# Kernel tuning notes

Hardware: AMD Instinct MI355X
Metric: run time of the kernel (lower is better)

Reference implementation:

```python
import jax, jax.numpy as jnp
import numpy as np

B, P, D = 256, 128, 768        # batch, property slots per sample, encoder hidden dim
E = 64                          # num_properties (number of adapter heads)
H = 256                         # adapter_hidden_dim
H2 = H // 2
O = 2                           # output_dim
LN_EPS = 1e-5
RES_W_ADPT, RES_W_BASE = 0.7, 0.3


def setup_inputs() -> dict:
    key = jax.random.key(0)
    ks = jax.random.split(key, 12)
    hidden_states = jax.random.normal(ks[0], (B, P, D), dtype=jnp.float32)
    base_output = jax.random.normal(ks[1], (B, P, O), dtype=jnp.float32)
    properties = jax.random.randint(ks[2], (B, P), 0, E, dtype=jnp.int64)
    mask = (jax.random.uniform(ks[3], (B, P)) > 0.1).astype(jnp.float32)
    # Stacked per-head adapter parameters (LayerNorm + 3 Linears per head)
    ln_g = jnp.ones((E, D), dtype=jnp.float32)
    ln_b = jnp.zeros((E, D), dtype=jnp.float32)
    W1 = jax.random.normal(ks[4], (E, D, H), dtype=jnp.float32) * (1.0 / np.sqrt(D))
    b1 = jnp.zeros((E, H), dtype=jnp.float32)
    W2 = jax.random.normal(ks[5], (E, H, H2), dtype=jnp.float32) * (1.0 / np.sqrt(H))
    b2 = jnp.zeros((E, H2), dtype=jnp.float32)
    W3 = jax.random.normal(ks[6], (E, H2, O), dtype=jnp.float32) * 0.01  # init std=0.01 per source
    b3 = jnp.zeros((E, O), dtype=jnp.float32)
    return {
        "hidden_states": hidden_states, "base_output": base_output,
        "properties": properties, "mask": mask,
        "ln_g": ln_g, "ln_b": ln_b, "W1": W1, "b1": b1,
        "W2": W2, "b2": b2, "W3": W3, "b3": b3,
    }


def reference(hidden_states, base_output, properties, mask,
              ln_g, ln_b, W1, b1, W2, b2, W3, b3):
    b, p, d = hidden_states.shape
    o = W3.shape[-1]
    x = hidden_states.reshape(-1, d)                        # [N, D]
    # LayerNorm statistics are head-independent; only gamma/beta differ per head
    mu = jnp.mean(x, axis=-1, keepdims=True)
    var = jnp.mean((x - mu) ** 2, axis=-1, keepdims=True)
    xhat = (x - mu) * jax.lax.rsqrt(var + LN_EPS)           # [N, D]
    flat_p = properties.reshape(-1)                         # [N]
    flat_m = mask.reshape(-1)                               # [N]

    def body(acc, inp):
        idx, g, bt, w1, bb1, w2, bb2, w3, bb3 = inp
        h = jax.nn.relu((xhat * g + bt) @ w1 + bb1)         # [N, H]  (dropout = identity in eval)
        h = jax.nn.relu(h @ w2 + bb2)                       # [N, H2]
        out = h @ w3 + bb3                                  # [N, O]
        sel = (flat_p == idx) & (flat_m > 0)
        return jnp.where(sel[:, None], out, acc), None

    e = W1.shape[0]
    acc0 = jnp.zeros((b * p, o), dtype=x.dtype)
    acc, _ = jax.lax.scan(
        body, acc0,
        (jnp.arange(e), ln_g, ln_b, W1, b1, W2, b2, W3, b3))
    out = acc.reshape(b, p, o)
    out = RES_W_ADPT * out + RES_W_BASE * base_output       # use_residual=True
    return out * mask[..., None]
```

## Files before the change

### kernel.cpp

```cpp
#include <hip/hip_runtime.h>
#include <stdint.h>

typedef unsigned short u16;
typedef unsigned int   u32;

#define NTOK   32768
#define GD     768
#define GH     256
#define GH2    128
#define GE     64

typedef __bf16 bf16x8 __attribute__((ext_vector_type(8)));
typedef float  f32x4  __attribute__((ext_vector_type(4)));
union Frag { uint4 u; bf16x8 b; };

__device__ __forceinline__ float bf2f(u16 h) {
  union { u32 u; float f; } v; v.u = ((u32)h) << 16; return v.f;
}
__device__ __forceinline__ u16 f2bf(float f) {
  union { float f; u32 u; } v; v.f = f;
  u32 r = (v.u + 0x7fffu + ((v.u >> 16) & 1u)) >> 16;
  return (u16)r;
}

__device__ __forceinline__ void async16(void* lds, const void* g) {
  __builtin_amdgcn_global_load_lds(
      (const __attribute__((address_space(1))) void*)g,
      (__attribute__((address_space(3))) void*)lds, 16, 0, 0);
}

__device__ __forceinline__ int getProp(const int* p32, int t, int is64) {
  return is64 ? p32[2 * t] : p32[t];
}

static const size_t OFF_Y    = 0;
static const size_t OFF_W1T  = 50331648;
static const size_t OFF_W2T  = 75497472;
static const size_t OFF_TOK  = 79691776;
static const size_t OFF_META = 79822848;

__global__ void setup_kernel(const int* __restrict__ prop, const float* __restrict__ mask,
                             u32* __restrict__ outz, int* __restrict__ counts2d,
                             int* __restrict__ cursors_p, int* __restrict__ flagp) {
  __shared__ int h[GE];
  __shared__ int vOr;
  const int b = blockIdx.x;
  const int tid = threadIdx.x;
  outz[b * 512 + tid] = 0u;
  outz[b * 512 + 256 + tid] = 0u;
  if (b < 4) cursors_p[b * 256 + tid] = 0;
  if (tid < GE) h[tid] = 0;
  if (tid == 0) vOr = 0;
  __syncthreads();
  int v = prop[2 * tid + 1] | prop[2 * (tid + 256) + 1];
  if (v) atomicOr(&vOr, 1);
  __syncthreads();
  const int is64 = (vOr == 0) ? 1 : 0;
  if (b == 0 && tid == 0) *flagp = is64;
  const int t = b * 256 + tid;
  if (mask[t] > 0.f) atomicAdd(&h[getProp(prop, t, is64)], 1);
  __syncthreads();
  if (tid < GE) counts2d[b * GE + tid] = h[tid];
}

__global__ void transpose_w1(const float* __restrict__ in, u16* __restrict__ out) {
  __shared__ u16 tl[64][260];
  const int bid = blockIdx.x;
  const int e  = bid / 12, r = bid % 12;
  const int d0 = (r / 4) * 256, h0 = (r % 4) * 64;
  const int tid = threadIdx.x;
  const size_t inMat = (size_t)e * GD * GH;
  const size_t outMat = (size_t)e * GH * GD;
  const int h_l = (tid & 15) * 4, d_l = tid >> 4;
#pragma unroll
  for (int dd = 0; dd < 16; ++dd) {
    const int d = d_l + dd * 16;
    float4 v = *(const float4*)(in + inMat + (size_t)(d0 + d) * GH + h0 + h_l);
    tl[h_l + 0][d] = f2bf(v.x);
    tl[h_l + 1][d] = f2bf(v.y);
    tl[h_l + 2][d] = f2bf(v.z);
    tl[h_l + 3][d] = f2bf(v.w);
  }
  __syncthreads();
  const int wv = tid >> 6, ln = tid & 63;
#pragma unroll
  for (int hh = 0; hh < 16; ++hh) {
    const int h = wv * 16 + hh;
    *(uint2*)(out + outMat + (size_t)(h0 + h) * GD + d0 + ln * 4) =
        *(const uint2*)&tl[h][ln * 4];
  }
}

__global__ void transpose_kernel(const float* __restrict__ in, u16* __restrict__ out,
                                 int R, int C, int tilesC) {
  __shared__ u16 tile[32][33];
  const int tilesPerMat = (R >> 5) * tilesC;
  const int e  = blockIdx.x / tilesPerMat;
  const int t  = blockIdx.x % tilesPerMat;
  const int tr = t / tilesC, tc = t % tilesC;
  const size_t mat = (size_t)e * R * C;
  const int tx = threadIdx.x & 31, ty = threadIdx.x >> 5;
  const int r0 = tr * 32, c0 = tc * 32;
#pragma unroll
  for (int i = 0; i < 32; i += 8)
    tile[ty + i][tx] = f2bf(in[mat + (size_t)(r0 + ty + i) * C + c0 + tx]);
  __syncthreads();
#pragma unroll
  for (int i = 0; i < 32; i += 8)
    out[mat + (size_t)(c0 + ty + i) * R + r0 + tx] = tile[tx][ty + i];
}

__global__ void ln_kernel(const float* __restrict__ hs, const float* __restrict__ g,
                          const float* __restrict__ bta, const int* __restrict__ prop,
                          u16* __restrict__ y, const int* __restrict__ flag) {
  const int wv = threadIdx.x >> 6, ln = threadIdx.x & 63;
  const int t = blockIdx.x * 4 + wv;
  const float* x = hs + (size_t)t * GD;
  float v[12];
  float s = 0.f, sq = 0.f;
#pragma unroll
  for (int c = 0; c < 3; ++c) {
    float4 u = *(const float4*)(x + c * 256 + ln * 4);
    v[c*4+0] = u.x; v[c*4+1] = u.y; v[c*4+2] = u.z; v[c*4+3] = u.w;
    s  += u.x + u.y + u.z + u.w;
    sq += u.x*u.x + u.y*u.y + u.z*u.z + u.w*u.w;
  }
#pragma unroll
  for (int d = 1; d < 64; d <<= 1) { s += __shfl_xor(s, d); sq += __shfl_xor(sq, d); }
  const float mu = s * (1.f / 768.f);
  const float rstd = rsqrtf(sq * (1.f / 768.f) - mu * mu + 1e-5f);
  const int p = getProp(prop, t, *flag);
  const float* gp = g + (size_t)p * GD;
  const float* bp = bta + (size_t)p * GD;
  u16* yp = y + (size_t)t * GD;
#pragma unroll
  for (int c = 0; c < 3; ++c) {
    float4 ug = *(const float4*)(gp + c * 256 + ln * 4);
    float4 ub = *(const float4*)(bp + c * 256 + ln * 4);
    float y0 = (v[c*4+0] - mu) * rstd * ug.x + ub.x;
    float y1 = (v[c*4+1] - mu) * rstd * ug.y + ub.y;
    float y2 = (v[c*4+2] - mu) * rstd * ug.z + ub.z;
    float y3 = (v[c*4+3] - mu) * rstd * ug.w + ub.w;
    uint2 o;
    o.x = (u32)f2bf(y0) | ((u32)f2bf(y1) << 16);
    o.y = (u32)f2bf(y2) | ((u32)f2bf(y3) << 16);
    *(uint2*)(yp + c * 256 + ln * 4) = o;
  }
}

__global__ void scan_kernel(const int* __restrict__ counts2d, int* __restrict__ offsets,
                            int* __restrict__ tileHead, int* __restrict__ tileRow,
                            int* __restrict__ nTilesPtr) {
  const int e = threadIdx.x;
  int c = 0;
  for (int b = 0; b < 128; ++b) c += counts2d[b * GE + e];
  int inc = c;
#pragma unroll
  for (int d = 1; d < 64; d <<= 1) { int n = __shfl_up(inc, d); if (e >= d) inc += n; }
  const int off = inc - c;
  offsets[e] = off;
  if (e == 63) offsets[64] = inc;
  int ntile = (c + 127) >> 7;
  int inct = ntile;
#pragma unroll
  for (int d = 1; d < 64; d <<= 1) { int n = __shfl_up(inct, d); if (e >= d) inct += n; }
  const int tb = inct - ntile;
  for (int j = 0; j < ntile; ++j) { tileHead[tb + j] = e; tileRow[tb + j] = off + j * 128; }
  if (e == 63) *nTilesPtr = inct;
}

__global__ void scatter_kernel(const int* __restrict__ prop, const float* __restrict__ mask,
                               const int* __restrict__ offsets, int* __restrict__ cursors_p,
                               int* __restrict__ tokenIds, const int* __restrict__ flag) {
  __shared__ int h[GE];
  __shared__ int basebin[GE];
  const int tid = threadIdx.x;
  const int t = blockIdx.x * 256 + tid;
  if (tid < GE) h[tid] = 0;
  __syncthreads();
  int p = -1, rank = 0;
  if (mask[t] > 0.f) {
    p = getProp(prop, t, *flag);
    rank = atomicAdd(&h[p], 1);
  }
  __syncthreads();
  if (tid < GE && h[tid] > 0) basebin[tid] = atomicAdd(&cursors_p[tid * 16], h[tid]);
  __syncthreads();
  if (p >= 0) tokenIds[offsets[p] + basebin[p] + rank] = t;
}

__global__ __launch_bounds__(256, 2) void adapter_gemm(
    const u16* __restrict__ y, const u16* __restrict__ w1t, const u16* __restrict__ w2t,
    const float* __restrict__ b1, const float* __restrict__ b2,
    const float* __restrict__ w3, const float* __restrict__ b3,
    const float* __restrict__ base, const float* __restrict__ mask,
    const int* __restrict__ tokenIds, const int* __restrict__ offsets,
    const int* __restrict__ tileHead, const int* __restrict__ tileRow,
    const int* __restrict__ nTilesPtr, float* __restrict__ outp) {
  __shared__ union LU {
    u16 g1[4][4096];
    u16 h[17408];
  } uni;
  __shared__ u16 sB2[2][4096];
  __shared__ float sBias1[256];
  __shared__ float sBias2[128];
  __shared__ float sW3[2][128];
  __shared__ float sB3[2];
  __shared__ int   sTok[128];

  const int tid  = threadIdx.x;
  const int wv   = tid >> 6;
  const int l15  = tid & 15;
  const int quad = (tid & 63) >> 4;
  const int arow = tid >> 2;
  const int koff = (tid & 3) * 8;
  const f32x4 vzero = {0.f, 0.f, 0.f, 0.f};
  const int nt = *nTilesPtr;

  for (int tile = blockIdx.x; tile < nt; tile += gridDim.x) {
    __syncthreads();
    const int e  = tileHead[tile];
    const int rs = tileRow[tile];
    const int nRows = min(128, offsets[e + 1] - rs);

    if (tid < 128) sTok[tid] = tokenIds[rs + min(tid, nRows - 1)];
    sBias1[tid] = b1[e * GH + tid];
    if (tid < 128) sBias2[tid] = b2[e * GH2 + tid];
    { const int k = tid >> 1, o = tid & 1; sW3[o][k] = w3[e * GH2 * 2 + k * 2 + o]; }
    if (tid < 2) sB3[tid] = b3[e * 2 + tid];
    __syncthreads();

    const u16* yrow0 = y + (size_t)sTok[arow] * GD;
    const u16* yrow1 = y + (size_t)sTok[64 + arow] * GD;
    const u16* w1e = w1t + (size_t)e * GH * GD;
    const u16* w2e = w2t + (size_t)e * GH2 * GH;

    f32x4 acc2[8][2];
#pragma unroll
    for (int f = 0; f < 8; ++f)
#pragma unroll
      for (int g = 0; g < 2; ++g) acc2[f][g] = vzero;

    for (int c = 0; c < 2; ++c) {
      f32x4 acc1[8][2];
#pragma unroll
      for (int f = 0; f < 8; ++f)
#pragma unroll
        for (int g = 0; g < 2; ++g) acc1[f][g] = vzero;

      {
        u16* a = uni.g1[0]; u16* bb = uni.g1[2];
        async16(a + wv * 512,        yrow0 + koff);
        async16(a + 2048 + wv * 512, yrow1 + koff);
#pragma unroll
        for (int j = 0; j < 2; ++j)
          async16(bb + j * 2048 + wv * 512,
                  w1e + (size_t)(c * 128 + j * 64 + arow) * GD + koff);
      }

      for (int kt = 0; kt < 24; ++kt) {
        __syncthreads();
        if (kt + 1 < 24) {
          const int k0 = (kt + 1) * 32;
          const int par = (kt + 1) & 1;
          u16* a = uni.g1[par]; u16* bb = uni.g1[2 + par];
          async16(a + wv * 512,        yrow0 + k0 + koff);
          async16(a + 2048 + wv * 512, yrow1 + k0 + koff);
#pragma unroll
          for (int j = 0; j < 2; ++j)
            async16(bb + j * 2048 + wv * 512,
                    w1e + (size_t)(c * 128 + j * 64 + arow) * GD + k0 + koff);
        }
        const int par = kt & 1;
        const u16* a = uni.g1[par]; const u16* bb = uni.g1[2 + par];
        Frag fa[8], fb[2];
#pragma unroll
        for (int f = 0; f < 8; ++f)
          fa[f].u = *(const uint4*)&a[(f * 16 + l15) * 32 + quad * 8];
#pragma unroll
        for (int g = 0; g < 2; ++g)
          fb[g].u = *(const uint4*)&bb[(wv * 32 + g * 16 + l15) * 32 + quad * 8];
#pragma unroll
        for (int f = 0; f < 8; ++f)
#pragma unroll
          for (int g = 0; g < 2; ++g)
            acc1[f][g] = __builtin_amdgcn_mfma_f32_16x16x32_bf16(fa[f].b, fb[g].b, acc1[f][g], 0, 0, 0);
      }
      __syncthreads();

#pragma unroll
      for (int j = 0; j < 2; ++j)
        async16(sB2[0] + j * 2048 + wv * 512,
                w2e + (size_t)(j * 64 + arow) * GH + c * 128 + koff);

#pragma unroll
      for (int f = 0; f < 8; ++f)
#pragma unroll
        for (int g = 0; g < 2; ++g) {
          const int col = wv * 32 + g * 16 + l15;
          const float bias = sBias1[c * 128 + col];
#pragma unroll
          for (int r = 0; r < 4; ++r) {
            const int row = f * 16 + quad * 4 + r;
            uni.h[row * 136 + col] = f2bf(fmaxf(acc1[f][g][r] + bias, 0.f));
          }
        }

      for (int kt = 0; kt < 4; ++kt) {
        __syncthreads();
        if (kt + 1 < 4) {
          const int k0 = (kt + 1) * 32;
          const int par = (kt + 1) & 1;
#pragma unroll
          for (int j = 0; j < 2; ++j)
            async16(sB2[par] + j * 2048 + wv * 512,
                    w2e + (size_t)(j * 64 + arow) * GH + c * 128 + k0 + koff);
        }
        const int par = kt & 1;
        Frag fa2[8], fb2[2];
#pragma unroll
        for (int f = 0; f < 8; ++f)
          fa2[f].u = *(const uint4*)&uni.h[(f * 16 + l15) * 136 + kt * 32 + quad * 8];
#pragma unroll
        for (int g = 0; g < 2; ++g)
          fb2[g].u = *(const uint4*)&sB2[par][(wv * 32 + g * 16 + l15) * 32 + quad * 8];
#pragma unroll
        for (int f = 0; f < 8; ++f)
#pragma unroll
          for (int g = 0; g < 2; ++g)
            acc2[f][g] = __builtin_amdgcn_mfma_f32_16x16x32_bf16(fa2[f].b, fb2[g].b, acc2[f][g], 0, 0, 0);
      }
      __syncthreads();
    }

#pragma unroll
    for (int f = 0; f < 8; ++f)
#pragma unroll
      for (int g = 0; g < 2; ++g) {
        const int col = wv * 32 + g * 16 + l15;
        const float bias = sBias2[col];
#pragma unroll
        for (int r = 0; r < 4; ++r) {
          const int row = f * 16 + quad * 4 + r;
          uni.h[row * 136 + col] = f2bf(fmaxf(acc2[f][g][r] + bias, 0.f));
        }
      }
    __syncthreads();

    const int m = tid >> 1, o = tid & 1;
    if (m < nRows) {
      float a = sB3[o];
      const u16* h2row = &uni.h[m * 136];
#pragma unroll 16
      for (int k = 0; k < 128; ++k) a += bf2f(h2row[k]) * sW3[o][k];
      const int t = sTok[m];
      const float mk = mask[t];
      const float bs = base[t * 2 + o];
      outp[t * 2 + o] = (0.7f * a + 0.3f * bs) * mk;
    }
  }
}

extern "C" void kernel_launch(void* const* d_in, const int* in_sizes, int n_in,
                              void* d_out, int out_size, void* d_ws, size_t ws_size,
                              hipStream_t stream) {
  const float* hs   = (const float*)d_in[0];
  const float* base = (const float*)d_in[1];
  const int*   prop = (const int*)d_in[2];
  const float* mask = (const float*)d_in[3];
  const float* lng  = (const float*)d_in[4];
  const float* lnb  = (const float*)d_in[5];
  const float* W1   = (const float*)d_in[6];
  const float* b1   = (const float*)d_in[7];
  const float* W2   = (const float*)d_in[8];
  const float* b2   = (const float*)d_in[9];
  const float* W3   = (const float*)d_in[10];
  const float* b3   = (const float*)d_in[11];

  char* ws = (char*)d_ws;
  u16* y    = (u16*)(ws + OFF_Y);
  u16* w1t  = (u16*)(ws + OFF_W1T);
  u16* w2t  = (u16*)(ws + OFF_W2T);
  int* tok  = (int*)(ws + OFF_TOK);
  int* meta = (int*)(ws + OFF_META);
  int* counts2d  = meta;
  int* offsets   = meta + 8192;
  int* tileHead  = meta + 8320;
  int* tileRow   = meta + 8832;
  int* nTiles    = meta + 9344;
  int* propFlag  = meta + 9345;
  int* cursors_p = meta + 10240;

  setup_kernel<<<128, 256, 0, stream>>>(prop, mask, (u32*)d_out, counts2d,
                                        cursors_p, propFlag);
  transpose_w1<<<768, 256, 0, stream>>>(W1, w1t);
  transpose_kernel<<<64 * 8 * 4, 256, 0, stream>>>(W2, w2t, GH, GH2, 4);
  ln_kernel<<<NTOK / 4, 256, 0, stream>>>(hs, lng, lnb, prop, y, propFlag);
  scan_kernel<<<1, 64, 0, stream>>>(counts2d, offsets, tileHead, tileRow, nTiles);
  scatter_kernel<<<NTOK / 256, 256, 0, stream>>>(prop, mask, offsets, cursors_p, tok, propFlag);
  adapter_gemm<<<512, 256, 0, stream>>>(y, w1t, w2t, b1, b2, W3, b3, base, mask,
                                        tok, offsets, tileHead, tileRow, nTiles,
                                        (float*)d_out);
}
```

Measured before the change: 284.8 us.

## Use 64-row token tiles with full 256-wide hidden layer per tile

Tiles shrink from 128 to 64 tokens per head, and each tile now computes the full 256-wide first hidden layer in one pass instead of two 128-column chunks. The LDS staging layout changes to k-major fragments, the grid grows to 640 blocks, and the metadata offsets move to fit the larger tile table. The aim is less padding waste on partial tiles and more tiles to spread across CUs. The cost is that W1 and W2 are reloaded per 64 tokens instead of per 128, which doubles weight traffic per token.

```diff
diff --git a/kernel.cpp b/kernel.cpp
--- a/kernel.cpp
+++ b/kernel.cpp
@@ -160,12 +160,12 @@
   const int off = inc - c;
   offsets[e] = off;
   if (e == 63) offsets[64] = inc;
-  int ntile = (c + 127) >> 7;
+  int ntile = (c + 63) >> 6;
   int inct = ntile;
 #pragma unroll
   for (int d = 1; d < 64; d <<= 1) { int n = __shfl_up(inct, d); if (e >= d) inct += n; }
   const int tb = inct - ntile;
-  for (int j = 0; j < ntile; ++j) { tileHead[tb + j] = e; tileRow[tb + j] = off + j * 128; }
+  for (int j = 0; j < ntile; ++j) { tileHead[tb + j] = e; tileRow[tb + j] = off + j * 64; }
   if (e == 63) *nTilesPtr = inct;
 }
 
@@ -198,7 +198,7 @@
     const int* __restrict__ tileHead, const int* __restrict__ tileRow,
     const int* __restrict__ nTilesPtr, float* __restrict__ outp) {
   __shared__ union LU {
-    u16 g1[4][4096];
+    struct { u16 A[2][2048]; u16 B[2][8192]; } s;
     u16 h[17408];
   } uni;
   __shared__ u16 sB2[2][4096];
@@ -206,14 +206,13 @@
   __shared__ float sBias2[128];
   __shared__ float sW3[2][128];
   __shared__ float sB3[2];
-  __shared__ int   sTok[128];
+  __shared__ int   sTok[64];
 
   const int tid  = threadIdx.x;
   const int wv   = tid >> 6;
+  const int ln   = tid & 63;
   const int l15  = tid & 15;
   const int quad = (tid & 63) >> 4;
-  const int arow = tid >> 2;
-  const int koff = (tid & 3) * 8;
   const f32x4 vzero = {0.f, 0.f, 0.f, 0.f};
   const int nt = *nTilesPtr;
 
@@ -221,120 +220,112 @@
     __syncthreads();
     const int e  = tileHead[tile];
     const int rs = tileRow[tile];
-    const int nRows = min(128, offsets[e + 1] - rs);
-
-    if (tid < 128) sTok[tid] = tokenIds[rs + min(tid, nRows - 1)];
+    const int nRows = min(64, offsets[e + 1] - rs);
+
+    if (tid < 64) sTok[tid] = tokenIds[rs + min(tid, nRows - 1)];
     sBias1[tid] = b1[e * GH + tid];
     if (tid < 128) sBias2[tid] = b2[e * GH2 + tid];
     { const int k = tid >> 1, o = tid & 1; sW3[o][k] = w3[e * GH2 * 2 + k * 2 + o]; }
     if (tid < 2) sB3[tid] = b3[e * 2 + tid];
     __syncthreads();
 
-    const u16* yrow0 = y + (size_t)sTok[arow] * GD;
-    const u16* yrow1 = y + (size_t)sTok[64 + arow] * GD;
+    const u16* yrow = y + (size_t)sTok[ln] * GD;
     const u16* w1e = w1t + (size_t)e * GH * GD;
     const u16* w2e = w2t + (size_t)e * GH2 * GH;
 
-    f32x4 acc2[8][2];
-#pragma unroll
-    for (int f = 0; f < 8; ++f)
+    f32x4 acc1[4][4];
+#pragma unroll
+    for (int f = 0; f < 4; ++f)
+#pragma unroll
+      for (int g = 0; g < 4; ++g) acc1[f][g] = vzero;
+
+    {
+      async16(uni.s.A[0] + wv * 512, yrow + wv * 8);
+#pragma unroll
+      for (int j = 0; j < 4; ++j)
+        async16(uni.s.B[0] + wv * 2048 + j * 512,
+                w1e + (size_t)(j * 64 + ln) * GD + wv * 8);
+    }
+
+    for (int kt = 0; kt < 24; ++kt) {
+      __syncthreads();
+      if (kt + 1 < 24) {
+        const int k0 = (kt + 1) * 32;
+        const int par = (kt + 1) & 1;
+        async16(uni.s.A[par] + wv * 512, yrow + k0 + wv * 8);
+#pragma unroll
+        for (int j = 0; j < 4; ++j)
+          async16(uni.s.B[par] + wv * 2048 + j * 512,
+                  w1e + (size_t)(j * 64 + ln) * GD + k0 + wv * 8);
+      }
+      const int par = kt & 1;
+      Frag fa[4], fb[4];
+#pragma unroll
+      for (int f = 0; f < 4; ++f)
+        fa[f].u = *(const uint4*)&uni.s.A[par][quad * 512 + (f * 16 + l15) * 8];
+#pragma unroll
+      for (int g = 0; g < 4; ++g)
+        fb[g].u = *(const uint4*)&uni.s.B[par][quad * 2048 + (wv * 64 + g * 16 + l15) * 8];
+#pragma unroll
+      for (int f = 0; f < 4; ++f)
+#pragma unroll
+        for (int g = 0; g < 4; ++g)
+          acc1[f][g] = __builtin_amdgcn_mfma_f32_16x16x32_bf16(fa[f].b, fb[g].b, acc1[f][g], 0, 0, 0);
+    }
+    __syncthreads();
+
+#pragma unroll
+    for (int j = 0; j < 2; ++j)
+      async16(sB2[0] + wv * 1024 + j * 512,
+              w2e + (size_t)(j * 64 + ln) * GH + wv * 8);
+
+#pragma unroll
+    for (int f = 0; f < 4; ++f)
+#pragma unroll
+      for (int g = 0; g < 4; ++g) {
+        const int col = wv * 64 + g * 16 + l15;
+        const float bias = sBias1[col];
+#pragma unroll
+        for (int r = 0; r < 4; ++r) {
+          const int row = f * 16 + quad * 4 + r;
+          uni.h[row * 264 + col] = f2bf(fmaxf(acc1[f][g][r] + bias, 0.f));
+        }
+      }
+
+    f32x4 acc2[4][2];
+#pragma unroll
+    for (int f = 0; f < 4; ++f)
 #pragma unroll
       for (int g = 0; g < 2; ++g) acc2[f][g] = vzero;
 
-    for (int c = 0; c < 2; ++c) {
-      f32x4 acc1[8][2];
-#pragma unroll
-      for (int f = 0; f < 8; ++f)
-#pragma unroll
-        for (int g = 0; g < 2; ++g) acc1[f][g] = vzero;
-
-      {
-        u16* a = uni.g1[0]; u16* bb = uni.g1[2];
-        async16(a + wv * 512,        yrow0 + koff);
-        async16(a + 2048 + wv * 512, yrow1 + koff);
+    for (int kt = 0; kt < 8; ++kt) {
+      __syncthreads();
+      if (kt + 1 < 8) {
+        const int k0 = (kt + 1) * 32;
+        const int par = (kt + 1) & 1;
 #pragma unroll
         for (int j = 0; j < 2; ++j)
-          async16(bb + j * 2048 + wv * 512,
-                  w1e + (size_t)(c * 128 + j * 64 + arow) * GD + koff);
+          async16(sB2[par] + wv * 1024 + j * 512,
+                  w2e + (size_t)(j * 64 + ln) * GH + k0 + wv * 8);
       }
-
-      for (int kt = 0; kt < 24; ++kt) {
-        __syncthreads();
-        if (kt + 1 < 24) {
-          const int k0 = (kt + 1) * 32;
-          const int par = (kt + 1) & 1;
-          u16* a = uni.g1[par]; u16* bb = uni.g1[2 + par];
-          async16(a + wv * 512,        yrow0 + k0 + koff);
-          async16(a + 2048 + wv * 512, yrow1 + k0 + koff);
-#pragma unroll
-          for (int j = 0; j < 2; ++j)
-            async16(bb + j * 2048 + wv * 512,
-                    w1e + (size_t)(c * 128 + j * 64 + arow) * GD + k0 + koff);
-        }
-        const int par = kt & 1;
-        const u16* a = uni.g1[par]; const u16* bb = uni.g1[2 + par];
-        Frag fa[8], fb[2];
-#pragma unroll
-        for (int f = 0; f < 8; ++f)
-          fa[f].u = *(const uint4*)&a[(f * 16 + l15) * 32 + quad * 8];
+      const int par = kt & 1;
+      Frag fa2[4], fb2[2];
+#pragma unroll
+      for (int f = 0; f < 4; ++f)
+        fa2[f].u = *(const uint4*)&uni.h[(f * 16 + l15) * 264 + kt * 32 + quad * 8];
+#pragma unroll
+      for (int g = 0; g < 2; ++g)
+        fb2[g].u = *(const uint4*)&sB2[par][quad * 1024 + (wv * 32 + g * 16 + l15) * 8];
+#pragma unroll
+      for (int f = 0; f < 4; ++f)
 #pragma unroll
         for (int g = 0; g < 2; ++g)
-          fb[g].u = *(const uint4*)&bb[(wv * 32 + g * 16 + l15) * 32 + quad * 8];
-#pragma unroll
-        for (int f = 0; f < 8; ++f)
-#pragma unroll
-          for (int g = 0; g < 2; ++g)
-            acc1[f][g] = __builtin_amdgcn_mfma_f32_16x16x32_bf16(fa[f].b, fb[g].b, acc1[f][g], 0, 0, 0);
-      }
-      __syncthreads();
-
-#pragma unroll
-      for (int j = 0; j < 2; ++j)
-        async16(sB2[0] + j * 2048 + wv * 512,
-                w2e + (size_t)(j * 64 + arow) * GH + c * 128 + koff);
-
-#pragma unroll
-      for (int f = 0; f < 8; ++f)
-#pragma unroll
-        for (int g = 0; g < 2; ++g) {
-          const int col = wv * 32 + g * 16 + l15;
-          const float bias = sBias1[c * 128 + col];
-#pragma unroll
-          for (int r = 0; r < 4; ++r) {
-            const int row = f * 16 + quad * 4 + r;
-            uni.h[row * 136 + col] = f2bf(fmaxf(acc1[f][g][r] + bias, 0.f));
-          }
-        }
-
-      for (int kt = 0; kt < 4; ++kt) {
-        __syncthreads();
-        if (kt + 1 < 4) {
-          const int k0 = (kt + 1) * 32;
-          const int par = (kt + 1) & 1;
-#pragma unroll
-          for (int j = 0; j < 2; ++j)
-            async16(sB2[par] + j * 2048 + wv * 512,
-                    w2e + (size_t)(j * 64 + arow) * GH + c * 128 + k0 + koff);
-        }
-        const int par = kt & 1;
-        Frag fa2[8], fb2[2];
-#pragma unroll
-        for (int f = 0; f < 8; ++f)
-          fa2[f].u = *(const uint4*)&uni.h[(f * 16 + l15) * 136 + kt * 32 + quad * 8];
-#pragma unroll
-        for (int g = 0; g < 2; ++g)
-          fb2[g].u = *(const uint4*)&sB2[par][(wv * 32 + g * 16 + l15) * 32 + quad * 8];
-#pragma unroll
-        for (int f = 0; f < 8; ++f)
-#pragma unroll
-          for (int g = 0; g < 2; ++g)
-            acc2[f][g] = __builtin_amdgcn_mfma_f32_16x16x32_bf16(fa2[f].b, fb2[g].b, acc2[f][g], 0, 0, 0);
-      }
-      __syncthreads();
+          acc2[f][g] = __builtin_amdgcn_mfma_f32_16x16x32_bf16(fa2[f].b, fb2[g].b, acc2[f][g], 0, 0, 0);
     }
-
-#pragma unroll
-    for (int f = 0; f < 8; ++f)
+    __syncthreads();
+
+#pragma unroll
+    for (int f = 0; f < 4; ++f)
 #pragma unroll
       for (int g = 0; g < 2; ++g) {
         const int col = wv * 32 + g * 16 + l15;
@@ -342,7 +333,7 @@
 #pragma unroll
         for (int r = 0; r < 4; ++r) {
           const int row = f * 16 + quad * 4 + r;
-          uni.h[row * 136 + col] = f2bf(fmaxf(acc2[f][g][r] + bias, 0.f));
+          uni.h[row * 130 + col] = f2bf(fmaxf(acc2[f][g][r] + bias, 0.f));
         }
       }
     __syncthreads();
@@ -350,7 +341,7 @@
     const int m = tid >> 1, o = tid & 1;
     if (m < nRows) {
       float a = sB3[o];
-      const u16* h2row = &uni.h[m * 136];
+      const u16* h2row = &uni.h[m * 130];
 #pragma unroll 16
       for (int k = 0; k < 128; ++k) a += bf2f(h2row[k]) * sW3[o][k];
       const int t = sTok[m];
@@ -386,10 +377,10 @@
   int* counts2d  = meta;
   int* offsets   = meta + 8192;
   int* tileHead  = meta + 8320;
-  int* tileRow   = meta + 8832;
-  int* nTiles    = meta + 9344;
-  int* propFlag  = meta + 9345;
-  int* cursors_p = meta + 10240;
+  int* tileRow   = meta + 9344;
+  int* nTiles    = meta + 10368;
+  int* propFlag  = meta + 10369;
+  int* cursors_p = meta + 10432;
 
   setup_kernel<<<128, 256, 0, stream>>>(prop, mask, (u32*)d_out, counts2d,
                                         cursors_p, propFlag);
@@ -398,7 +389,7 @@
   ln_kernel<<<NTOK / 4, 256, 0, stream>>>(hs, lng, lnb, prop, y, propFlag);
   scan_kernel<<<1, 64, 0, stream>>>(counts2d, offsets, tileHead, tileRow, nTiles);
   scatter_kernel<<<NTOK / 256, 256, 0, stream>>>(prop, mask, offsets, cursors_p, tok, propFlag);
-  adapter_gemm<<<512, 256, 0, stream>>>(y, w1t, w2t, b1, b2, W3, b3, base, mask,
+  adapter_gemm<<<640, 256, 0, stream>>>(y, w1t, w2t, b1, b2, W3, b3, base, mask,
                                         tok, offsets, tileHead, tileRow, nTiles,
                                         (float*)d_out);
 }
```

After: 283.0 us. No clear change (-0.6%).
